# Optimization experiments

Measured on AMD Instinct MI355X. Metric: run time of the kernel, lower is better.

## Reference

```python
import jax, jax.numpy as jnp
import numpy as np

D_MODEL = 512
N_HEADS = 8
D_FF = 2048
WINDOW = 32
EPS = 1e-5


def _layernorm(x, g, b):
    mu = jnp.mean(x, axis=-1, keepdims=True)
    var = jnp.mean(jnp.square(x - mu), axis=-1, keepdims=True)
    return (x - mu) * jax.lax.rsqrt(var + EPS) * g + b


def setup_inputs() -> dict:
    key = jax.random.key(0)
    ks = jax.random.split(key, 12)
    B, S, D = 8, 8192, D_MODEL
    s = 0.02
    return {
        "x": jax.random.normal(ks[0], (B, S, D), dtype=jnp.float32),
        "Wq": jax.random.normal(ks[1], (D, D), dtype=jnp.float32) * s,
        "bq": jnp.zeros((D,), jnp.float32),
        "Wk": jax.random.normal(ks[2], (D, D), dtype=jnp.float32) * s,
        "bk": jnp.zeros((D,), jnp.float32),
        "Wv": jax.random.normal(ks[3], (D, D), dtype=jnp.float32) * s,
        "bv": jnp.zeros((D,), jnp.float32),
        "Wo": jax.random.normal(ks[4], (D, D), dtype=jnp.float32) * s,
        "bo": jnp.zeros((D,), jnp.float32),
        "g1": jnp.ones((D,), jnp.float32),
        "be1": jnp.zeros((D,), jnp.float32),
        "W1": jax.random.normal(ks[5], (D, D_FF), dtype=jnp.float32) * s,
        "b1": jnp.zeros((D_FF,), jnp.float32),
        "W2": jax.random.normal(ks[6], (D_FF, D), dtype=jnp.float32) * s,
        "b2": jnp.zeros((D,), jnp.float32),
        "g2": jnp.ones((D,), jnp.float32),
        "be2": jnp.zeros((D,), jnp.float32),
    }


def reference(x, Wq, bq, Wk, bk, Wv, bv, Wo, bo, g1, be1, W1, b1, W2, b2, g2, be2):
    B, S, D = x.shape
    H, W = N_HEADS, WINDOW
    dh = D // H
    nW = S // W

    def split(t):  # [B,S,D] -> [B,nW,W,H,dh]
        return t.reshape(B, nW, W, H, dh)

    q = split(x @ Wq + bq)
    k = split(x @ Wk + bk)
    v = split(x @ Wv + bv)

    # block-local (non-overlapping window) attention: [B,H,nW,W,W]
    scores = jnp.einsum('bnqhd,bnkhd->bhnqk', q, k) / jnp.sqrt(jnp.float32(dh))
    attn = jax.nn.softmax(scores, axis=-1)
    o = jnp.einsum('bhnqk,bnkhd->bnqhd', attn, v).reshape(B, S, D)
    attn_out = o @ Wo + bo

    x = _layernorm(x + attn_out, g1, be1)
    ff = jax.nn.relu(x @ W1 + b1) @ W2 + b2
    x = _layernorm(x + ff, g2, be2)
    return x
```

## Files before the change

### kernel.cpp

```cpp
#include <hip/hip_runtime.h>

typedef unsigned int uint;
typedef unsigned short ushort;

typedef __bf16 bf16x8 __attribute__((ext_vector_type(8)));
typedef float f32x4 __attribute__((ext_vector_type(4)));

__device__ __forceinline__ float bflo(uint u) { return __uint_as_float(u << 16); }
__device__ __forceinline__ float bfhi(uint u) { return __uint_as_float(u & 0xffff0000u); }
__device__ __forceinline__ ushort f2bf(float f) {
  uint u = __float_as_uint(f);
  u += 0x7fffu + ((u >> 16) & 1u);
  return (ushort)(u >> 16);
}
__device__ __forceinline__ uint pack2(float lo, float hi) {
  return (uint)f2bf(lo) | ((uint)f2bf(hi) << 16);
}

__global__ __launch_bounds__(256) void cvt_f32_bf16(
    const float* __restrict__ in, ushort* __restrict__ out)
{
  const long i = ((long)blockIdx.x * 256 + threadIdx.x) * 8;
  float4 a = *(const float4*)(in + i);
  float4 b = *(const float4*)(in + i + 4);
  uint4 r;
  r.x = pack2(a.x, a.y); r.y = pack2(a.z, a.w);
  r.z = pack2(b.x, b.y); r.w = pack2(b.z, b.w);
  *(uint4*)(out + i) = r;
}

__global__ __launch_bounds__(256) void transpose_wf(
    const float* __restrict__ in, ushort* __restrict__ out, int R, int Ccols)
{
  __shared__ float tile[32][33];
  const int tx = threadIdx.x, ty = threadIdx.y;
  const int c0 = blockIdx.x * 32, r0 = blockIdx.y * 32;
#pragma unroll
  for (int j = 0; j < 32; j += 8)
    tile[ty + j][tx] = in[(long)(r0 + ty + j) * Ccols + (c0 + tx)];
  __syncthreads();
#pragma unroll
  for (int j = 0; j < 32; j += 8)
    out[(long)(c0 + ty + j) * R + (r0 + tx)] = f2bf(tile[tx][ty + j]);
}

#define BM 128
#define BN 128
#define BKK 64
#define CSTR 136
#define FSTR 132

__global__ __launch_bounds__(256, 2) void gemm_bt(
    const ushort* __restrict__ A, const ushort* __restrict__ Bt,
    const float* __restrict__ bias, void* __restrict__ Cv,
    int M, int N, int K, int relu, int out_f32)
{
  __shared__ ushort smem[17408];
  ushort* As = smem;
  ushort* Bs = smem + BM * BKK;
  const int t = threadIdx.x;
  const int w = t >> 6, l = t & 63;
  const int quad = l >> 4, l16 = l & 15;
  const int wm = w & 1, wn = w >> 1;

  const int gx = gridDim.x;
  int bid = blockIdx.y * gx + blockIdx.x;
  const int nwg = gx * gridDim.y;
  if ((nwg & 7) == 0) bid = (bid & 7) * (nwg >> 3) + (bid >> 3);
  const long m0 = (long)(bid / gx) * BM;
  const long n0 = (long)(bid % gx) * BN;

  const int srow = l >> 3;
  const int scol = (l & 7) * 8;

  f32x4 acc[4][4];
#pragma unroll
  for (int i = 0; i < 4; ++i)
#pragma unroll
    for (int j = 0; j < 4; ++j)
      acc[i][j] = f32x4{0.f, 0.f, 0.f, 0.f};

  for (int k0 = 0; k0 < K; k0 += BKK) {
#pragma unroll
    for (int i = 0; i < 4; ++i) {
      const int chunk = w * 4 + i;
      const int row = chunk * 8 + srow;
      const ushort* ga = A + (m0 + row) * (long)K + k0 + scol;
      const ushort* gb = Bt + (n0 + row) * (long)K + k0 + scol;
      __builtin_amdgcn_global_load_lds(
          (const __attribute__((address_space(1))) uint*)ga,
          (__attribute__((address_space(3))) uint*)(As + chunk * 512), 16, 0, 0);
      __builtin_amdgcn_global_load_lds(
          (const __attribute__((address_space(1))) uint*)gb,
          (__attribute__((address_space(3))) uint*)(Bs + chunk * 512), 16, 0, 0);
    }
    __syncthreads();
#pragma unroll
    for (int ks = 0; ks < 2; ++ks) {
      bf16x8 af[4], bfr[4];
#pragma unroll
      for (int im = 0; im < 4; ++im)
        af[im] = *(const bf16x8*)(As + (wm * 64 + im * 16 + l16) * BKK + ks * 32 + quad * 8);
#pragma unroll
      for (int in = 0; in < 4; ++in)
        bfr[in] = *(const bf16x8*)(Bs + (wn * 64 + in * 16 + l16) * BKK + ks * 32 + quad * 8);
#pragma unroll
      for (int im = 0; im < 4; ++im)
#pragma unroll
        for (int in = 0; in < 4; ++in)
          acc[im][in] = __builtin_amdgcn_mfma_f32_16x16x32_bf16(af[im], bfr[in], acc[im][in], 0, 0, 0);
    }
    __syncthreads();
  }

  if (!out_f32) {
    ushort* Ct = smem;
#pragma unroll
    for (int in = 0; in < 4; ++in) {
      const int cl = wn * 64 + in * 16 + l16;
      const float bv = bias[n0 + cl];
#pragma unroll
      for (int im = 0; im < 4; ++im) {
        const int rl = wm * 64 + im * 16 + quad * 4;
#pragma unroll
        for (int r = 0; r < 4; ++r) {
          float vv = acc[im][in][r] + bv;
          if (relu) vv = fmaxf(vv, 0.f);
          Ct[(rl + r) * CSTR + cl] = f2bf(vv);
        }
      }
    }
    __syncthreads();
    ushort* Cb = (ushort*)Cv;
#pragma unroll
    for (int it = 0; it < 8; ++it) {
      const int idx = it * 256 + t;
      const int row = idx >> 4, c16 = idx & 15;
      uint4 d = *(const uint4*)(Ct + row * CSTR + c16 * 8);
      *(uint4*)(Cb + (m0 + row) * (long)N + n0 + c16 * 8) = d;
    }
  } else {
    float* Cf4 = (float*)smem;
    float* Cg = (float*)Cv;
#pragma unroll
    for (int half = 0; half < 2; ++half) {
      if (wm == half) {
#pragma unroll
        for (int in = 0; in < 4; ++in) {
          const int cl = wn * 64 + in * 16 + l16;
          const float bv = bias[n0 + cl];
#pragma unroll
          for (int im = 0; im < 4; ++im) {
            const int rl = im * 16 + quad * 4;
#pragma unroll
            for (int r = 0; r < 4; ++r) {
              float vv = acc[im][in][r] + bv;
              if (relu) vv = fmaxf(vv, 0.f);
              Cf4[(rl + r) * FSTR + cl] = vv;
            }
          }
        }
      }
      __syncthreads();
#pragma unroll
      for (int it = 0; it < 8; ++it) {
        const int idx = it * 256 + t;
        const int row = idx >> 5, c4 = idx & 31;
        float4 d = *(const float4*)(Cf4 + row * FSTR + c4 * 4);
        *(float4*)(Cg + (m0 + half * 64 + row) * (long)N + n0 + c4 * 4) = d;
      }
      __syncthreads();
    }
  }
}

__global__ __launch_bounds__(256, 2) void attn_mfma(
    ushort* qo, const ushort* __restrict__ k, const ushort* __restrict__ v)
{
  __shared__ ushort kv[32 * 512];
  __shared__ ushort pbuf[8][32 * 72];
  const int t = threadIdx.x;
  const int w = t >> 6, l = t & 63;
  const int quad = l >> 4, l16 = l & 15;
  const long base = (long)blockIdx.x * (32 * 512);

#pragma unroll
  for (int i = 0; i < 8; ++i) {
    const int c = w * 8 + i;
    __builtin_amdgcn_global_load_lds(
        (const __attribute__((address_space(1))) uint*)(k + base + c * 512 + l * 8),
        (__attribute__((address_space(3))) uint*)(kv + c * 512), 16, 0, 0);
  }
  bf16x8 qf[2][2][2];
#pragma unroll
  for (int hh = 0; hh < 2; ++hh) {
    const int h = w * 2 + hh;
#pragma unroll
    for (int mt = 0; mt < 2; ++mt)
#pragma unroll
      for (int ks = 0; ks < 2; ++ks)
        qf[hh][mt][ks] = *(const bf16x8*)(qo + base + (mt * 16 + l16) * 512 + h * 64 + ks * 32 + quad * 8);
  }
  __syncthreads();

#pragma unroll
  for (int hh = 0; hh < 2; ++hh) {
    const int h = w * 2 + hh;
    f32x4 sc[2][2];
#pragma unroll
    for (int mt = 0; mt < 2; ++mt)
#pragma unroll
      for (int nt = 0; nt < 2; ++nt)
        sc[mt][nt] = f32x4{0.f, 0.f, 0.f, 0.f};
#pragma unroll
    for (int ks = 0; ks < 2; ++ks) {
      bf16x8 kb0 = *(const bf16x8*)(kv + (0 * 16 + l16) * 512 + h * 64 + ks * 32 + quad * 8);
      bf16x8 kb1 = *(const bf16x8*)(kv + (1 * 16 + l16) * 512 + h * 64 + ks * 32 + quad * 8);
      sc[0][0] = __builtin_amdgcn_mfma_f32_16x16x32_bf16(qf[hh][0][ks], kb0, sc[0][0], 0, 0, 0);
      sc[0][1] = __builtin_amdgcn_mfma_f32_16x16x32_bf16(qf[hh][0][ks], kb1, sc[0][1], 0, 0, 0);
      sc[1][0] = __builtin_amdgcn_mfma_f32_16x16x32_bf16(qf[hh][1][ks], kb0, sc[1][0], 0, 0, 0);
      sc[1][1] = __builtin_amdgcn_mfma_f32_16x16x32_bf16(qf[hh][1][ks], kb1, sc[1][1], 0, 0, 0);
    }
    ushort* pb = pbuf[w * 2 + hh];
#pragma unroll
    for (int mt = 0; mt < 2; ++mt) {
#pragma unroll
      for (int r = 0; r < 4; ++r) {
        float a = sc[mt][0][r] * 0.125f;
        float b = sc[mt][1][r] * 0.125f;
        float mx = fmaxf(a, b);
        mx = fmaxf(mx, __shfl_xor(mx, 1));
        mx = fmaxf(mx, __shfl_xor(mx, 2));
        mx = fmaxf(mx, __shfl_xor(mx, 4));
        mx = fmaxf(mx, __shfl_xor(mx, 8));
        float ea = __expf(a - mx), eb = __expf(b - mx);
        float s = ea + eb;
        s += __shfl_xor(s, 1);
        s += __shfl_xor(s, 2);
        s += __shfl_xor(s, 4);
        s += __shfl_xor(s, 8);
        const float inv = 1.f / s;
        const int row = mt * 16 + quad * 4 + r;
        pb[row * 72 + 0 * 16 + l16] = f2bf(ea * inv);
        pb[row * 72 + 1 * 16 + l16] = f2bf(eb * inv);
      }
    }
  }
  __syncthreads();

#pragma unroll
  for (int i = 0; i < 8; ++i) {
    const int c = w * 8 + i;
    __builtin_amdgcn_global_load_lds(
        (const __attribute__((address_space(1))) uint*)(v + base + c * 512 + l * 8),
        (__attribute__((address_space(3))) uint*)(kv + c * 512), 16, 0, 0);
  }
  bf16x8 pf[2][2];
#pragma unroll
  for (int hh = 0; hh < 2; ++hh)
#pragma unroll
    for (int mt = 0; mt < 2; ++mt)
      pf[hh][mt] = *(const bf16x8*)(pbuf[w * 2 + hh] + (mt * 16 + l16) * 72 + quad * 8);
  __syncthreads();

#pragma unroll
  for (int hh = 0; hh < 2; ++hh) {
    const int h = w * 2 + hh;
    f32x4 oc[2][4];
#pragma unroll
    for (int mt = 0; mt < 2; ++mt)
#pragma unroll
      for (int nt = 0; nt < 4; ++nt)
        oc[mt][nt] = f32x4{0.f, 0.f, 0.f, 0.f};
#pragma unroll
    for (int nt = 0; nt < 4; ++nt) {
      bf16x8 bv;
#pragma unroll
      for (int j = 0; j < 8; ++j)
        bv[j] = ((const __bf16*)kv)[(quad * 8 + j) * 512 + h * 64 + nt * 16 + l16];
      oc[0][nt] = __builtin_amdgcn_mfma_f32_16x16x32_bf16(pf[hh][0], bv, oc[0][nt], 0, 0, 0);
      oc[1][nt] = __builtin_amdgcn_mfma_f32_16x16x32_bf16(pf[hh][1], bv, oc[1][nt], 0, 0, 0);
    }
    ushort* pb = pbuf[w * 2 + hh];
#pragma unroll
    for (int mt = 0; mt < 2; ++mt)
#pragma unroll
      for (int nt = 0; nt < 4; ++nt)
#pragma unroll
        for (int r = 0; r < 4; ++r)
          pb[(mt * 16 + quad * 4 + r) * 72 + nt * 16 + l16] = f2bf(oc[mt][nt][r]);
  }

#pragma unroll
  for (int i = 0; i < 8; ++i) {
    const int idx = i * 64 + l;
    const int hh = idx >> 8;
    const int row = (idx >> 3) & 31;
    const int c8 = idx & 7;
    uint4 d = *(const uint4*)(pbuf[w * 2 + hh] + row * 72 + c8 * 8);
    *(uint4*)(qo + base + row * 512 + (w * 2 + hh) * 64 + c8 * 8) = d;
  }
}

__global__ __launch_bounds__(256, 4) void ln1_res(
    const ushort* __restrict__ a, const ushort* __restrict__ b,
    const float* __restrict__ g, const float* __restrict__ be,
    ushort* __restrict__ out)
{
  const long row = (long)blockIdx.x * 4 + (threadIdx.x >> 6);
  const int lane = threadIdx.x & 63;
  const long off = row * 512 + lane * 8;
  uint4 ua = *(const uint4*)(a + off);
  uint4 ub = *(const uint4*)(b + off);
  float x[8];
  x[0] = bflo(ua.x) + bflo(ub.x); x[1] = bfhi(ua.x) + bfhi(ub.x);
  x[2] = bflo(ua.y) + bflo(ub.y); x[3] = bfhi(ua.y) + bfhi(ub.y);
  x[4] = bflo(ua.z) + bflo(ub.z); x[5] = bfhi(ua.z) + bfhi(ub.z);
  x[6] = bflo(ua.w) + bflo(ub.w); x[7] = bfhi(ua.w) + bfhi(ub.w);
  float sum = 0.f;
#pragma unroll
  for (int i = 0; i < 8; ++i) sum += x[i];
#pragma unroll
  for (int i = 1; i < 64; i <<= 1) sum += __shfl_xor(sum, i, 64);
  const float mu = sum * (1.0f / 512.0f);
  float vsum = 0.f;
#pragma unroll
  for (int i = 0; i < 8; ++i) { const float d = x[i] - mu; vsum += d * d; }
#pragma unroll
  for (int i = 1; i < 64; i <<= 1) vsum += __shfl_xor(vsum, i, 64);
  const float rs = rsqrtf(vsum * (1.0f / 512.0f) + 1e-5f);
  float4 g0 = *(const float4*)(g + lane * 8);
  float4 g1v = *(const float4*)(g + lane * 8 + 4);
  float4 e0 = *(const float4*)(be + lane * 8);
  float4 e1 = *(const float4*)(be + lane * 8 + 4);
  uint4 r;
  r.x = pack2((x[0] - mu) * rs * g0.x + e0.x, (x[1] - mu) * rs * g0.y + e0.y);
  r.y = pack2((x[2] - mu) * rs * g0.z + e0.z, (x[3] - mu) * rs * g0.w + e0.w);
  r.z = pack2((x[4] - mu) * rs * g1v.x + e1.x, (x[5] - mu) * rs * g1v.y + e1.y);
  r.w = pack2((x[6] - mu) * rs * g1v.z + e1.z, (x[7] - mu) * rs * g1v.w + e1.w);
  *(uint4*)(out + off) = r;
}

__global__ __launch_bounds__(256, 4) void ln2_res(
    const ushort* __restrict__ a, const float* bff,
    const float* __restrict__ g, const float* __restrict__ be,
    float* out)
{
  const long row = (long)blockIdx.x * 4 + (threadIdx.x >> 6);
  const int lane = threadIdx.x & 63;
  const long off = row * 512 + lane * 8;
  uint4 ua = *(const uint4*)(a + off);
  float4 fa = *(const float4*)(bff + off);
  float4 fb = *(const float4*)(bff + off + 4);
  float x[8];
  x[0] = bflo(ua.x) + fa.x; x[1] = bfhi(ua.x) + fa.y;
  x[2] = bflo(ua.y) + fa.z; x[3] = bfhi(ua.y) + fa.w;
  x[4] = bflo(ua.z) + fb.x; x[5] = bfhi(ua.z) + fb.y;
  x[6] = bflo(ua.w) + fb.z; x[7] = bfhi(ua.w) + fb.w;
  float sum = 0.f;
#pragma unroll
  for (int i = 0; i < 8; ++i) sum += x[i];
#pragma unroll
  for (int i = 1; i < 64; i <<= 1) sum += __shfl_xor(sum, i, 64);
  const float mu = sum * (1.0f / 512.0f);
  float vsum = 0.f;
#pragma unroll
  for (int i = 0; i < 8; ++i) { const float d = x[i] - mu; vsum += d * d; }
#pragma unroll
  for (int i = 1; i < 64; i <<= 1) vsum += __shfl_xor(vsum, i, 64);
  const float rs = rsqrtf(vsum * (1.0f / 512.0f) + 1e-5f);
  float4 g0 = *(const float4*)(g + lane * 8);
  float4 g1v = *(const float4*)(g + lane * 8 + 4);
  float4 e0 = *(const float4*)(be + lane * 8);
  float4 e1 = *(const float4*)(be + lane * 8 + 4);
  float4 r0, r1;
  r0.x = (x[0] - mu) * rs * g0.x + e0.x;
  r0.y = (x[1] - mu) * rs * g0.y + e0.y;
  r0.z = (x[2] - mu) * rs * g0.z + e0.z;
  r0.w = (x[3] - mu) * rs * g0.w + e0.w;
  r1.x = (x[4] - mu) * rs * g1v.x + e1.x;
  r1.y = (x[5] - mu) * rs * g1v.y + e1.y;
  r1.z = (x[6] - mu) * rs * g1v.z + e1.z;
  r1.w = (x[7] - mu) * rs * g1v.w + e1.w;
  *(float4*)(out + off) = r0;
  *(float4*)(out + off + 4) = r1;
}

extern "C" void kernel_launch(void* const* d_in, const int* in_sizes, int n_in,
                              void* d_out, int out_size, void* d_ws, size_t ws_size,
                              hipStream_t stream)
{
  const float* x   = (const float*)d_in[0];
  const float* Wq  = (const float*)d_in[1];
  const float* bq  = (const float*)d_in[2];
  const float* Wk  = (const float*)d_in[3];
  const float* bk  = (const float*)d_in[4];
  const float* Wv  = (const float*)d_in[5];
  const float* bv  = (const float*)d_in[6];
  const float* Wo  = (const float*)d_in[7];
  const float* bo  = (const float*)d_in[8];
  const float* g1  = (const float*)d_in[9];
  const float* be1 = (const float*)d_in[10];
  const float* W1  = (const float*)d_in[11];
  const float* b1  = (const float*)d_in[12];
  const float* W2  = (const float*)d_in[13];
  const float* b2  = (const float*)d_in[14];
  const float* g2  = (const float*)d_in[15];
  const float* be2 = (const float*)d_in[16];

  const long M = 65536;
  const size_t SZ = (size_t)M * 512;

  ushort* wsb = (ushort*)d_ws;
  ushort* xb  = wsb;
  ushort* R0  = wsb + SZ;
  ushort* Wqt = wsb + 2 * SZ;
  ushort* Wkt = Wqt + 512 * 512;
  ushort* Wvt = Wkt + 512 * 512;
  ushort* Wot = Wvt + 512 * 512;
  ushort* W1t = Wot + 512 * 512;
  ushort* W2t = W1t + 512 * 2048;

  ushort* outb = (ushort*)d_out;
  ushort* kb = outb;
  ushort* vb = outb + SZ;
  float* outf = (float*)d_out;

  dim3 tb(32, 8);
  transpose_wf<<<dim3(16, 16), tb, 0, stream>>>(Wq, Wqt, 512, 512);
  transpose_wf<<<dim3(16, 16), tb, 0, stream>>>(Wk, Wkt, 512, 512);
  transpose_wf<<<dim3(16, 16), tb, 0, stream>>>(Wv, Wvt, 512, 512);
  transpose_wf<<<dim3(16, 16), tb, 0, stream>>>(Wo, Wot, 512, 512);
  transpose_wf<<<dim3(64, 16), tb, 0, stream>>>(W1, W1t, 512, 2048);
  transpose_wf<<<dim3(16, 64), tb, 0, stream>>>(W2, W2t, 2048, 512);
  cvt_f32_bf16<<<dim3(16384), dim3(256), 0, stream>>>(x, xb);

  dim3 blk(256);
  gemm_bt<<<dim3(4, 512), blk, 0, stream>>>(xb, Wqt, bq, R0, 65536, 512, 512, 0, 0);
  gemm_bt<<<dim3(4, 512), blk, 0, stream>>>(xb, Wkt, bk, kb, 65536, 512, 512, 0, 0);
  gemm_bt<<<dim3(4, 512), blk, 0, stream>>>(xb, Wvt, bv, vb, 65536, 512, 512, 0, 0);
  attn_mfma<<<dim3(2048), blk, 0, stream>>>(R0, kb, vb);
  gemm_bt<<<dim3(4, 512), blk, 0, stream>>>(R0, Wot, bo, outb, 65536, 512, 512, 0, 0);
  ln1_res<<<dim3(16384), blk, 0, stream>>>(xb, outb, g1, be1, R0);
  for (int c = 0; c < 4; ++c) {
    const size_t rows0 = (size_t)c * 16384;
    gemm_bt<<<dim3(16, 128), blk, 0, stream>>>(R0 + rows0 * 512, W1t, b1, xb,
                                               16384, 2048, 512, 1, 0);
    gemm_bt<<<dim3(4, 128), blk, 0, stream>>>(xb, W2t, b2, outf + rows0 * 512,
                                              16384, 512, 2048, 0, 1);
  }
  ln2_res<<<dim3(16384), blk, 0, stream>>>(R0, outf, g2, be2, outf);
}
```

Baseline: 1.038 ms.

## Replace GEMM with 256x256 double-buffered 8-wave pipelined kernel with swizzled LDS

Replaces the 128x128 single-buffered GEMM with a 256x256-tile, 512-thread kernel. It double-buffers K tiles in LDS, XOR-swizzles the LDS layout to avoid bank conflicts, and interleaves global-to-LDS staging with quadrant-wise MFMA work behind explicit waitcnt and barriers, raising MFMA priority with setprio. The goal is to hide load latency and raise arithmetic intensity per tile. The cost is 128KB of LDS and many more accumulator registers, which may limit occupancy and adds hand-tuned synchronisation that is easy to get wrong.

```diff
diff --git a/kernel.cpp b/kernel.cpp
--- a/kernel.cpp
+++ b/kernel.cpp
@@ -5,6 +5,9 @@
 
 typedef __bf16 bf16x8 __attribute__((ext_vector_type(8)));
 typedef float f32x4 __attribute__((ext_vector_type(4)));
+
+#define AS1 __attribute__((address_space(1)))
+#define AS3 __attribute__((address_space(3)))
 
 __device__ __forceinline__ float bflo(uint u) { return __uint_as_float(u << 16); }
 __device__ __forceinline__ float bfhi(uint u) { return __uint_as_float(u & 0xffff0000u); }
@@ -44,134 +47,214 @@
     out[(long)(c0 + ty + j) * R + (r0 + tx)] = f2bf(tile[tx][ty + j]);
 }
 
-#define BM 128
-#define BN 128
-#define BKK 64
-#define CSTR 136
-#define FSTR 132
-
-__global__ __launch_bounds__(256, 2) void gemm_bt(
+__global__ __launch_bounds__(512, 2) void gemm256(
     const ushort* __restrict__ A, const ushort* __restrict__ Bt,
     const float* __restrict__ bias, void* __restrict__ Cv,
     int M, int N, int K, int relu, int out_f32)
 {
-  __shared__ ushort smem[17408];
-  ushort* As = smem;
-  ushort* Bs = smem + BM * BKK;
+  __shared__ ushort lds[65536];
   const int t = threadIdx.x;
   const int w = t >> 6, l = t & 63;
   const int quad = l >> 4, l16 = l & 15;
-  const int wm = w & 1, wn = w >> 1;
+  const int wm = w >> 2, wn = w & 3;
 
   const int gx = gridDim.x;
   int bid = blockIdx.y * gx + blockIdx.x;
   const int nwg = gx * gridDim.y;
   if ((nwg & 7) == 0) bid = (bid & 7) * (nwg >> 3) + (bid >> 3);
-  const long m0 = (long)(bid / gx) * BM;
-  const long n0 = (long)(bid % gx) * BN;
-
-  const int srow = l >> 3;
-  const int scol = (l & 7) * 8;
-
-  f32x4 acc[4][4];
-#pragma unroll
-  for (int i = 0; i < 4; ++i)
+  const long m0 = (long)(bid / gx) * 256;
+  const long n0 = (long)(bid % gx) * 256;
+
+  const int lr = l >> 3;
+  const int lc = l & 7;
+  const int swc = lc ^ lr;
+  int arow[2][2], brow[2][2];
+#pragma unroll
+  for (int s = 0; s < 2; ++s) {
+    const int o = w * 2 + s;
+    arow[0][s] = (o >> 3) * 128 + (o & 7) * 8;
+    arow[1][s] = arow[0][s] + 64;
+    brow[0][s] = (o >> 2) * 64 + (o & 3) * 8;
+    brow[1][s] = brow[0][s] + 32;
+  }
+  uint aoff[2][2], boff[2][2];
+#pragma unroll
+  for (int X = 0; X < 2; ++X)
+#pragma unroll
+    for (int s = 0; s < 2; ++s) {
+      aoff[X][s] = (uint)((m0 + arow[X][s] + lr) * (long)K + swc * 8);
+      boff[X][s] = (uint)((n0 + brow[X][s] + lr) * (long)K + swc * 8);
+    }
+
+#define STAGE_A(X, kt) do { \
+    __builtin_amdgcn_global_load_lds((const AS1 uint*)(A + aoff[X][0] + (uint)(kt) * 64u), \
+        (AS3 uint*)(lds + (((kt) & 1) << 14) + arow[X][0] * 64), 16, 0, 0); \
+    __builtin_amdgcn_global_load_lds((const AS1 uint*)(A + aoff[X][1] + (uint)(kt) * 64u), \
+        (AS3 uint*)(lds + (((kt) & 1) << 14) + arow[X][1] * 64), 16, 0, 0); } while (0)
+#define STAGE_B(Y, kt) do { \
+    __builtin_amdgcn_global_load_lds((const AS1 uint*)(Bt + boff[Y][0] + (uint)(kt) * 64u), \
+        (AS3 uint*)(lds + 32768 + (((kt) & 1) << 14) + brow[Y][0] * 64), 16, 0, 0); \
+    __builtin_amdgcn_global_load_lds((const AS1 uint*)(Bt + boff[Y][1] + (uint)(kt) * 64u), \
+        (AS3 uint*)(lds + 32768 + (((kt) & 1) << 14) + brow[Y][1] * 64), 16, 0, 0); } while (0)
+
+  const int rswz0 = ((0 + quad) ^ (l16 & 7)) * 8;
+  const int rswz1 = ((4 + quad) ^ (l16 & 7)) * 8;
+  const int abase = wm * 8192 + l16 * 64;
+  const int bbase = 32768 + wn * 4096 + l16 * 64;
+
+  bf16x8 af[4][2], b0v[2][2], b1v[2][2];
+
+#define LDA(mh, p) do { \
+  _Pragma("unroll") for (int i_ = 0; i_ < 4; ++i_) { \
+    af[i_][0] = *(const bf16x8*)(lds + ((p) << 14) + abase + ((mh) * 4 + i_) * 1024 + rswz0); \
+    af[i_][1] = *(const bf16x8*)(lds + ((p) << 14) + abase + ((mh) * 4 + i_) * 1024 + rswz1); } } while (0)
+#define LDB(nh, p, bq) do { \
+  _Pragma("unroll") for (int j_ = 0; j_ < 2; ++j_) { \
+    bq[j_][0] = *(const bf16x8*)(lds + ((p) << 14) + bbase + ((nh) * 2 + j_) * 1024 + rswz0); \
+    bq[j_][1] = *(const bf16x8*)(lds + ((p) << 14) + bbase + ((nh) * 2 + j_) * 1024 + rswz1); } } while (0)
+#define MFMAQ(mh, nh, bq) do { \
+  __builtin_amdgcn_s_setprio(1); \
+  _Pragma("unroll") for (int ks_ = 0; ks_ < 2; ++ks_) \
+  _Pragma("unroll") for (int i_ = 0; i_ < 4; ++i_) \
+  _Pragma("unroll") for (int j_ = 0; j_ < 2; ++j_) \
+    acc[(mh) * 4 + i_][(nh) * 2 + j_] = __builtin_amdgcn_mfma_f32_16x16x32_bf16( \
+        af[i_][ks_], bq[j_][ks_], acc[(mh) * 4 + i_][(nh) * 2 + j_], 0, 0, 0); \
+  __builtin_amdgcn_s_setprio(0); } while (0)
+#define BAR() __builtin_amdgcn_s_barrier()
+#define WAITLGKM() asm volatile("s_waitcnt lgkmcnt(0)" ::: "memory")
+#define WAITVM(n) asm volatile("s_waitcnt vmcnt(" #n ")" ::: "memory")
+
+  f32x4 acc[8][4];
+#pragma unroll
+  for (int i = 0; i < 8; ++i)
 #pragma unroll
     for (int j = 0; j < 4; ++j)
       acc[i][j] = f32x4{0.f, 0.f, 0.f, 0.f};
 
-  for (int k0 = 0; k0 < K; k0 += BKK) {
-#pragma unroll
-    for (int i = 0; i < 4; ++i) {
-      const int chunk = w * 4 + i;
-      const int row = chunk * 8 + srow;
-      const ushort* ga = A + (m0 + row) * (long)K + k0 + scol;
-      const ushort* gb = Bt + (n0 + row) * (long)K + k0 + scol;
-      __builtin_amdgcn_global_load_lds(
-          (const __attribute__((address_space(1))) uint*)ga,
-          (__attribute__((address_space(3))) uint*)(As + chunk * 512), 16, 0, 0);
-      __builtin_amdgcn_global_load_lds(
-          (const __attribute__((address_space(1))) uint*)gb,
-          (__attribute__((address_space(3))) uint*)(Bs + chunk * 512), 16, 0, 0);
-    }
-    __syncthreads();
-#pragma unroll
-    for (int ks = 0; ks < 2; ++ks) {
-      bf16x8 af[4], bfr[4];
-#pragma unroll
-      for (int im = 0; im < 4; ++im)
-        af[im] = *(const bf16x8*)(As + (wm * 64 + im * 16 + l16) * BKK + ks * 32 + quad * 8);
-#pragma unroll
-      for (int in = 0; in < 4; ++in)
-        bfr[in] = *(const bf16x8*)(Bs + (wn * 64 + in * 16 + l16) * BKK + ks * 32 + quad * 8);
-#pragma unroll
-      for (int im = 0; im < 4; ++im)
-#pragma unroll
-        for (int in = 0; in < 4; ++in)
-          acc[im][in] = __builtin_amdgcn_mfma_f32_16x16x32_bf16(af[im], bfr[in], acc[im][in], 0, 0, 0);
-    }
-    __syncthreads();
+  const int NT = K >> 6;
+  const int NIT = NT >> 1;
+
+  STAGE_A(0, 0); STAGE_B(1, 0); STAGE_A(1, 0); STAGE_B(0, 0);
+  STAGE_A(0, 1); STAGE_B(1, 1);
+  WAITVM(4);
+  BAR();
+
+  for (int it = 0; it < NIT; ++it) {
+    const int t1 = 2 * it + 1, t2 = 2 * it + 2, t3 = 2 * it + 3;
+    const bool more = (t2 < NT);
+    LDA(0, 0); LDB(0, 0, b0v);
+    STAGE_A(1, t1);
+    BAR(); WAITLGKM();
+    MFMAQ(0, 0, b0v);
+    BAR();
+    LDB(1, 0, b1v);
+    STAGE_B(0, t1);
+    BAR(); WAITLGKM();
+    MFMAQ(0, 1, b1v);
+    BAR();
+    LDA(1, 0);
+    if (more) STAGE_A(0, t2);
+    BAR(); WAITLGKM();
+    MFMAQ(1, 1, b1v);
+    BAR();
+    LDB(0, 0, b0v);
+    if (more) STAGE_B(1, t2);
+    BAR(); WAITLGKM();
+    MFMAQ(1, 0, b0v);
+    if (more) { WAITVM(4); } else { WAITVM(0); }
+    BAR();
+    LDA(0, 1); LDB(0, 1, b0v);
+    if (more) STAGE_A(1, t2);
+    BAR(); WAITLGKM();
+    MFMAQ(0, 0, b0v);
+    BAR();
+    LDB(1, 1, b1v);
+    if (more) STAGE_B(0, t2);
+    BAR(); WAITLGKM();
+    MFMAQ(0, 1, b1v);
+    BAR();
+    LDA(1, 1);
+    if (t3 < NT) STAGE_A(0, t3);
+    BAR(); WAITLGKM();
+    MFMAQ(1, 1, b1v);
+    BAR();
+    LDB(0, 1, b0v);
+    if (t3 < NT) STAGE_B(1, t3);
+    BAR(); WAITLGKM();
+    MFMAQ(1, 0, b0v);
+    if (more) { WAITVM(4); } else { WAITVM(0); }
+    BAR();
   }
 
   if (!out_f32) {
-    ushort* Ct = smem;
-#pragma unroll
-    for (int in = 0; in < 4; ++in) {
-      const int cl = wn * 64 + in * 16 + l16;
-      const float bv = bias[n0 + cl];
-#pragma unroll
-      for (int im = 0; im < 4; ++im) {
-        const int rl = wm * 64 + im * 16 + quad * 4;
-#pragma unroll
-        for (int r = 0; r < 4; ++r) {
-          float vv = acc[im][in][r] + bv;
-          if (relu) vv = fmaxf(vv, 0.f);
-          Ct[(rl + r) * CSTR + cl] = f2bf(vv);
-        }
-      }
-    }
-    __syncthreads();
     ushort* Cb = (ushort*)Cv;
 #pragma unroll
-    for (int it = 0; it < 8; ++it) {
-      const int idx = it * 256 + t;
-      const int row = idx >> 4, c16 = idx & 15;
-      uint4 d = *(const uint4*)(Ct + row * CSTR + c16 * 8);
-      *(uint4*)(Cb + (m0 + row) * (long)N + n0 + c16 * 8) = d;
-    }
-  } else {
-    float* Cf4 = (float*)smem;
-    float* Cg = (float*)Cv;
-#pragma unroll
-    for (int half = 0; half < 2; ++half) {
-      if (wm == half) {
+    for (int hf = 0; hf < 2; ++hf) {
+      if (wm == hf) {
 #pragma unroll
         for (int in = 0; in < 4; ++in) {
           const int cl = wn * 64 + in * 16 + l16;
           const float bv = bias[n0 + cl];
 #pragma unroll
-          for (int im = 0; im < 4; ++im) {
-            const int rl = im * 16 + quad * 4;
+          for (int im = 0; im < 8; ++im)
 #pragma unroll
             for (int r = 0; r < 4; ++r) {
               float vv = acc[im][in][r] + bv;
               if (relu) vv = fmaxf(vv, 0.f);
-              Cf4[(rl + r) * FSTR + cl] = vv;
+              lds[(im * 16 + quad * 4 + r) * 264 + cl] = f2bf(vv);
             }
-          }
         }
       }
       __syncthreads();
 #pragma unroll
-      for (int it = 0; it < 8; ++it) {
-        const int idx = it * 256 + t;
-        const int row = idx >> 5, c4 = idx & 31;
-        float4 d = *(const float4*)(Cf4 + row * FSTR + c4 * 4);
-        *(float4*)(Cg + (m0 + half * 64 + row) * (long)N + n0 + c4 * 4) = d;
+      for (int it2 = 0; it2 < 8; ++it2) {
+        const int idx = it2 * 512 + t;
+        const int row = idx >> 5, c16 = idx & 31;
+        uint4 d = *(const uint4*)(lds + row * 264 + c16 * 8);
+        *(uint4*)(Cb + (m0 + hf * 128 + row) * (long)N + n0 + c16 * 8) = d;
       }
       __syncthreads();
     }
-  }
+  } else {
+    float* Cg = (float*)Cv;
+    float* Cf = (float*)lds;
+#pragma unroll
+    for (int p = 0; p < 4; ++p) {
+      if (wm == (p >> 1)) {
+        const int imh = p & 1;
+#pragma unroll
+        for (int in = 0; in < 4; ++in) {
+          const int cl = wn * 64 + in * 16 + l16;
+          const float bv = bias[n0 + cl];
+#pragma unroll
+          for (int i = 0; i < 4; ++i)
+#pragma unroll
+            for (int r = 0; r < 4; ++r) {
+              float vv = acc[imh * 4 + i][in][r] + bv;
+              if (relu) vv = fmaxf(vv, 0.f);
+              Cf[(i * 16 + quad * 4 + r) * 260 + cl] = vv;
+            }
+        }
+      }
+      __syncthreads();
+#pragma unroll
+      for (int it2 = 0; it2 < 8; ++it2) {
+        const int idx = it2 * 512 + t;
+        const int row = idx >> 6, c4 = idx & 63;
+        float4 d = *(const float4*)(Cf + row * 260 + c4 * 4);
+        *(float4*)(Cg + (m0 + p * 64 + row) * (long)N + n0 + c4 * 4) = d;
+      }
+      __syncthreads();
+    }
+  }
+#undef STAGE_A
+#undef STAGE_B
+#undef LDA
+#undef LDB
+#undef MFMAQ
+#undef BAR
+#undef WAITLGKM
+#undef WAITVM
 }
 
 __global__ __launch_bounds__(256, 2) void attn_mfma(
@@ -188,8 +271,8 @@
   for (int i = 0; i < 8; ++i) {
     const int c = w * 8 + i;
     __builtin_amdgcn_global_load_lds(
-        (const __attribute__((address_space(1))) uint*)(k + base + c * 512 + l * 8),
-        (__attribute__((address_space(3))) uint*)(kv + c * 512), 16, 0, 0);
+        (const AS1 uint*)(k + base + c * 512 + l * 8),
+        (AS3 uint*)(kv + c * 512), 16, 0, 0);
   }
   bf16x8 qf[2][2][2];
 #pragma unroll
@@ -252,8 +335,8 @@
   for (int i = 0; i < 8; ++i) {
     const int c = w * 8 + i;
     __builtin_amdgcn_global_load_lds(
-        (const __attribute__((address_space(1))) uint*)(v + base + c * 512 + l * 8),
-        (__attribute__((address_space(3))) uint*)(kv + c * 512), 16, 0, 0);
+        (const AS1 uint*)(v + base + c * 512 + l * 8),
+        (AS3 uint*)(kv + c * 512), 16, 0, 0);
   }
   bf16x8 pf[2][2];
 #pragma unroll
@@ -435,19 +518,19 @@
   transpose_wf<<<dim3(16, 64), tb, 0, stream>>>(W2, W2t, 2048, 512);
   cvt_f32_bf16<<<dim3(16384), dim3(256), 0, stream>>>(x, xb);
 
-  dim3 blk(256);
-  gemm_bt<<<dim3(4, 512), blk, 0, stream>>>(xb, Wqt, bq, R0, 65536, 512, 512, 0, 0);
-  gemm_bt<<<dim3(4, 512), blk, 0, stream>>>(xb, Wkt, bk, kb, 65536, 512, 512, 0, 0);
-  gemm_bt<<<dim3(4, 512), blk, 0, stream>>>(xb, Wvt, bv, vb, 65536, 512, 512, 0, 0);
-  attn_mfma<<<dim3(2048), blk, 0, stream>>>(R0, kb, vb);
-  gemm_bt<<<dim3(4, 512), blk, 0, stream>>>(R0, Wot, bo, outb, 65536, 512, 512, 0, 0);
-  ln1_res<<<dim3(16384), blk, 0, stream>>>(xb, outb, g1, be1, R0);
+  dim3 blk(512);
+  gemm256<<<dim3(2, 256), blk, 0, stream>>>(xb, Wqt, bq, R0, 65536, 512, 512, 0, 0);
+  gemm256<<<dim3(2, 256), blk, 0, stream>>>(xb, Wkt, bk, kb, 65536, 512, 512, 0, 0);
+  gemm256<<<dim3(2, 256), blk, 0, stream>>>(xb, Wvt, bv, vb, 65536, 512, 512, 0, 0);
+  attn_mfma<<<dim3(2048), dim3(256), 0, stream>>>(R0, kb, vb);
+  gemm256<<<dim3(2, 256), blk, 0, stream>>>(R0, Wot, bo, outb, 65536, 512, 512, 0, 0);
+  ln1_res<<<dim3(16384), dim3(256), 0, stream>>>(xb, outb, g1, be1, R0);
   for (int c = 0; c < 4; ++c) {
     const size_t rows0 = (size_t)c * 16384;
-    gemm_bt<<<dim3(16, 128), blk, 0, stream>>>(R0 + rows0 * 512, W1t, b1, xb,
-                                               16384, 2048, 512, 1, 0);
-    gemm_bt<<<dim3(4, 128), blk, 0, stream>>>(xb, W2t, b2, outf + rows0 * 512,
-                                              16384, 512, 2048, 0, 1);
-  }
-  ln2_res<<<dim3(16384), blk, 0, stream>>>(R0, outf, g2, be2, outf);
-}
+    gemm256<<<dim3(8, 64), blk, 0, stream>>>(R0 + rows0 * 512, W1t, b1, xb,
+                                             16384, 2048, 512, 1, 0);
+    gemm256<<<dim3(2, 64), blk, 0, stream>>>(xb, W2t, b2, outf + rows0 * 512,
+                                             16384, 512, 2048, 0, 1);
+  }
+  ln2_res<<<dim3(16384), dim3(256), 0, stream>>>(R0, outf, g2, be2, outf);
+}
```

Result: no change. 1.046 ms (+0.8%).
